# Kernel tuning notes

Hardware: AMD Instinct MI355X
Metric: run time of the kernel (lower is better)

The kernel has to match this reference:

```python
import jax, jax.numpy as jnp
import numpy as np

CHUNK = 1024  # chunk over N to avoid materializing the full [B,N,M] distance matrix


def _min_dists(xyz1, xyz2):
    """For each point in xyz1 [B,N,3], squared L2 distance to nearest point in xyz2 [B,M,3].
    Returns [B,N]. Computed in chunks of N to bound peak memory."""
    B, N, _ = xyz1.shape
    y2 = jnp.sum(xyz2 * xyz2, axis=-1)  # [B,M]
    n_chunks = N // CHUNK
    # [n_chunks, B, CHUNK, 3]
    xc = jnp.transpose(xyz1.reshape(B, n_chunks, CHUNK, 3), (1, 0, 2, 3))

    def chunk_min(x):  # x: [B,CHUNK,3]
        x2 = jnp.sum(x * x, axis=-1)  # [B,CHUNK]
        xy = jnp.einsum('bcd,bmd->bcm', x, xyz2)  # [B,CHUNK,M]
        d = x2[:, :, None] + y2[:, None, :] - 2.0 * xy
        return jnp.min(d, axis=-1)  # [B,CHUNK]

    mins = jax.lax.map(chunk_min, xc)  # [n_chunks, B, CHUNK]
    return jnp.transpose(mins, (1, 0, 2)).reshape(B, N)


def setup_inputs() -> dict:
    key = jax.random.key(0)
    k1, k2 = jax.random.split(key)
    xyz1 = jax.random.normal(k1, (8, 8192, 3), dtype=jnp.float32)
    xyz2 = jax.random.normal(k2, (8, 8192, 3), dtype=jnp.float32)
    return {"xyz1": xyz1, "xyz2": xyz2}


def reference(xyz1, xyz2):
    # ChamferDistanceL2.forward with ignore_zeros=False and batch>1:
    # only dist1 (xyz1 -> nearest in xyz2) is used; return its mean.
    dist1 = _min_dists(xyz1, xyz2)  # [B,N]
    return jnp.mean(dist1)
```

## Files before the change

kernel.cpp:

```cpp
#include <hip/hip_runtime.h>

typedef _Float16 v8h __attribute__((ext_vector_type(8)));
typedef float v16f __attribute__((ext_vector_type(16)));

#define BB 8
#define NN 8192
#define MM 8192
#define SPLITM 8
#define JT_PER_CHUNK 32
#define NI 2
#define TPB 256

#define AFRAG_OFF 0
#define BFRAG_OFF (8 * 256 * 64 * 16)
#define PMINS_OFF (2 * BFRAG_OFF)


__global__ __launch_bounds__(256) void pack_a(const float* __restrict__ xyz2,
                                              v8h* __restrict__ afrag,
                                              float* __restrict__ out) {
    int gid = blockIdx.x * 256 + threadIdx.x;
    if (gid == 0) out[0] = 0.0f;
    int lane = gid & 63;
    int jt = (gid >> 6) & 255;
    int b = gid >> 14;
    int j = jt * 32 + (lane & 31);
    int khalf = lane >> 5;
    const float* p = xyz2 + ((size_t)b * MM + j) * 3;
    _Float16 h0 = (_Float16)p[0], h1 = (_Float16)p[1], h2 = (_Float16)p[2];
    float y0 = (float)h0, y1 = (float)h1, y2v = (float)h2;
    float s = fmaf(y0, y0, fmaf(y1, y1, y2v * y2v));
    _Float16 shi = (_Float16)s;
    _Float16 slo = (_Float16)(s - (float)shi);
    v8h v = {0, 0, 0, 0, 0, 0, 0, 0};
    if (khalf == 0) {
        v[0] = h0; v[1] = h1; v[2] = h2;
        v[3] = shi; v[4] = slo;
        v[5] = (_Float16)1.0f; v[6] = (_Float16)1.0f;
    }
    afrag[gid] = v;
}

__global__ __launch_bounds__(256) void pack_b(const float* __restrict__ xyz1,
                                              v8h* __restrict__ bfrag) {
    int gid = blockIdx.x * 256 + threadIdx.x;
    int lane = gid & 63;
    int it = (gid >> 6) & 255;
    int b = gid >> 14;
    int i = it * 32 + (lane & 31);
    int khalf = lane >> 5;
    const float* p = xyz1 + ((size_t)b * NN + i) * 3;
    _Float16 h0 = (_Float16)p[0], h1 = (_Float16)p[1], h2 = (_Float16)p[2];
    float x0 = (float)h0, x1 = (float)h1, x2v = (float)h2;
    float s = fmaf(x0, x0, fmaf(x1, x1, x2v * x2v));
    _Float16 shi = (_Float16)s;
    _Float16 slo = (_Float16)(s - (float)shi);
    v8h v = {0, 0, 0, 0, 0, 0, 0, 0};
    if (khalf == 0) {
        v[0] = (_Float16)(-2.0f * x0);
        v[1] = (_Float16)(-2.0f * x1);
        v[2] = (_Float16)(-2.0f * x2v);
        v[3] = (_Float16)1.0f; v[4] = (_Float16)1.0f;
        v[5] = shi; v[6] = slo;
    }
    bfrag[gid] = v;
}

__global__ __launch_bounds__(TPB, 4) void chamfer_min_mfma(const v8h* __restrict__ afrag,
                                                           const v8h* __restrict__ bfrag,
                                                           float* __restrict__ pmins) {
    __shared__ v8h aLds[JT_PER_CHUNK * 64];

    int ig4    = blockIdx.x & 31;
    int jchunk = (blockIdx.x >> 5) & 7;
    int b      = blockIdx.x >> 8;
    int wid  = threadIdx.x >> 6;
    int lane = threadIdx.x & 63;

    {
        const uint4* src = (const uint4*)(afrag + ((size_t)b * 256 + jchunk * JT_PER_CHUNK) * 64);
        uint4* dst = (uint4*)aLds;
#pragma unroll
        for (int r = 0; r < JT_PER_CHUNK * 64 / TPB; ++r)
            dst[r * TPB + threadIdx.x] = src[r * TPB + threadIdx.x];
    }

    int it0 = (ig4 * 4 + wid) * NI;
    v8h b0 = bfrag[((size_t)b * 256 + it0 + 0) * 64 + lane];
    v8h b1 = bfrag[((size_t)b * 256 + it0 + 1) * 64 + lane];

    __syncthreads();

    const v16f zc = {0, 0, 0, 0, 0, 0, 0, 0, 0, 0, 0, 0, 0, 0, 0, 0};
    float m0 = 1e30f, m1 = 1e30f;

#pragma unroll 2
    for (int jt = 0; jt < JT_PER_CHUNK; ++jt) {
        v8h a = aLds[jt * 64 + lane];
        v16f c0 = __builtin_amdgcn_mfma_f32_32x32x16_f16(a, b0, zc, 0, 0, 0);
        v16f c1 = __builtin_amdgcn_mfma_f32_32x32x16_f16(a, b1, zc, 0, 0, 0);
#pragma unroll
        for (int r = 0; r < 16; r += 4) {
            m0 = fminf(m0, fminf(fminf(c0[r], c0[r + 1]), fminf(c0[r + 2], c0[r + 3])));
            m1 = fminf(m1, fminf(fminf(c1[r], c1[r + 1]), fminf(c1[r + 2], c1[r + 3])));
        }
    }

    m0 = fminf(m0, __shfl_xor(m0, 32));
    m1 = fminf(m1, __shfl_xor(m1, 32));

    int half = lane >> 5;
    int i = (it0 + half) * 32 + (lane & 31);
    float mv = half ? m1 : m0;
    pmins[(size_t)jchunk * (BB * NN) + (size_t)b * NN + i] = mv;
}

__global__ __launch_bounds__(256) void chamfer_reduce(const float* __restrict__ pmins,
                                                      float* __restrict__ out) {
    int i = blockIdx.x * 256 + threadIdx.x;
    float m = pmins[i];
#pragma unroll
    for (int sp = 1; sp < SPLITM; ++sp)
        m = fminf(m, pmins[(size_t)sp * (BB * NN) + i]);
    float s = m;
#pragma unroll
    for (int off = 32; off > 0; off >>= 1) s += __shfl_down(s, off);
    __shared__ float ls[4];
    int lane = threadIdx.x & 63, wv = threadIdx.x >> 6;
    if (lane == 0) ls[wv] = s;
    __syncthreads();
    if (threadIdx.x == 0) {
        float t = (ls[0] + ls[1]) + (ls[2] + ls[3]);
        atomicAdd(out, t * (1.0f / (float)(BB * NN)));
    }
}

extern "C" void kernel_launch(void* const* d_in, const int* in_sizes, int n_in,
                              void* d_out, int out_size, void* d_ws, size_t ws_size,
                              hipStream_t stream) {
    const float* xyz1 = (const float*)d_in[0];
    const float* xyz2 = (const float*)d_in[1];
    float* out = (float*)d_out;
    v8h* afrag = (v8h*)((char*)d_ws + AFRAG_OFF);
    v8h* bfrag = (v8h*)((char*)d_ws + BFRAG_OFF);
    float* pmins = (float*)((char*)d_ws + PMINS_OFF);

    pack_a<<<(BB * 256 * 64) / 256, 256, 0, stream>>>(xyz2, afrag, out);
    pack_b<<<(BB * 256 * 64) / 256, 256, 0, stream>>>(xyz1, bfrag);
    chamfer_min_mfma<<<BB * SPLITM * 32, TPB, 0, stream>>>(afrag, bfrag, pmins);
    chamfer_reduce<<<(BB * NN) / 256, 256, 0, stream>>>(pmins, out);
}
```

Measured before the change: 87.34 us.

## Fuse packing, MFMA min search and reduction into a single mega-kernel

```diff
diff --git a/kernel.cpp b/kernel.cpp
--- a/kernel.cpp
+++ b/kernel.cpp
@@ -6,133 +6,128 @@
 #define BB 8
 #define NN 8192
 #define MM 8192
-#define SPLITM 8
-#define JT_PER_CHUNK 32
-#define NI 2
-#define TPB 256
-
-#define AFRAG_OFF 0
-#define BFRAG_OFF (8 * 256 * 64 * 16)
-#define PMINS_OFF (2 * BFRAG_OFF)
+#define NCHUNK 8
+#define JTC 32
+#define CPTS (JTC * 32)
+#define TPB 128
+#define PPT (CPTS / TPB)
 
 
-__global__ __launch_bounds__(256) void pack_a(const float* __restrict__ xyz2,
-                                              v8h* __restrict__ afrag,
-                                              float* __restrict__ out) {
-    int gid = blockIdx.x * 256 + threadIdx.x;
-    if (gid == 0) out[0] = 0.0f;
-    int lane = gid & 63;
-    int jt = (gid >> 6) & 255;
-    int b = gid >> 14;
-    int j = jt * 32 + (lane & 31);
-    int khalf = lane >> 5;
-    const float* p = xyz2 + ((size_t)b * MM + j) * 3;
-    _Float16 h0 = (_Float16)p[0], h1 = (_Float16)p[1], h2 = (_Float16)p[2];
+__device__ __forceinline__ v8h cvt_a(float x, float y, float z) {
+    _Float16 h0 = (_Float16)x, h1 = (_Float16)y, h2 = (_Float16)z;
     float y0 = (float)h0, y1 = (float)h1, y2v = (float)h2;
     float s = fmaf(y0, y0, fmaf(y1, y1, y2v * y2v));
     _Float16 shi = (_Float16)s;
     _Float16 slo = (_Float16)(s - (float)shi);
-    v8h v = {0, 0, 0, 0, 0, 0, 0, 0};
-    if (khalf == 0) {
-        v[0] = h0; v[1] = h1; v[2] = h2;
-        v[3] = shi; v[4] = slo;
-        v[5] = (_Float16)1.0f; v[6] = (_Float16)1.0f;
-    }
-    afrag[gid] = v;
+    v8h v = {h0, h1, h2, shi, slo, (_Float16)1.0f, (_Float16)1.0f, (_Float16)0.0f};
+    return v;
 }
 
-__global__ __launch_bounds__(256) void pack_b(const float* __restrict__ xyz1,
-                                              v8h* __restrict__ bfrag) {
-    int gid = blockIdx.x * 256 + threadIdx.x;
-    int lane = gid & 63;
-    int it = (gid >> 6) & 255;
-    int b = gid >> 14;
-    int i = it * 32 + (lane & 31);
-    int khalf = lane >> 5;
-    const float* p = xyz1 + ((size_t)b * NN + i) * 3;
-    _Float16 h0 = (_Float16)p[0], h1 = (_Float16)p[1], h2 = (_Float16)p[2];
-    float x0 = (float)h0, x1 = (float)h1, x2v = (float)h2;
-    float s = fmaf(x0, x0, fmaf(x1, x1, x2v * x2v));
-    _Float16 shi = (_Float16)s;
-    _Float16 slo = (_Float16)(s - (float)shi);
-    v8h v = {0, 0, 0, 0, 0, 0, 0, 0};
-    if (khalf == 0) {
-        v[0] = (_Float16)(-2.0f * x0);
-        v[1] = (_Float16)(-2.0f * x1);
-        v[2] = (_Float16)(-2.0f * x2v);
-        v[3] = (_Float16)1.0f; v[4] = (_Float16)1.0f;
-        v[5] = shi; v[6] = slo;
-    }
-    bfrag[gid] = v;
-}
+__global__ __launch_bounds__(TPB, 1) void chamfer_mega(const float* __restrict__ xyz1,
+                                                       const float* __restrict__ xyz2,
+                                                       float* __restrict__ out) {
+    __shared__ v8h aLds[2][JTC * 64];
+    __shared__ float ls[2];
 
-__global__ __launch_bounds__(TPB, 4) void chamfer_min_mfma(const v8h* __restrict__ afrag,
-                                                           const v8h* __restrict__ bfrag,
-                                                           float* __restrict__ pmins) {
-    __shared__ v8h aLds[JT_PER_CHUNK * 64];
-
-    int ig4    = blockIdx.x & 31;
-    int jchunk = (blockIdx.x >> 5) & 7;
-    int b      = blockIdx.x >> 8;
-    int wid  = threadIdx.x >> 6;
-    int lane = threadIdx.x & 63;
+    int ig = blockIdx.x & 63;
+    int b  = blockIdx.x >> 6;
+    int t  = threadIdx.x;
+    int wid = t >> 6;
+    int lane = t & 63;
+    int laneq = lane & 31;
+    int half = lane >> 5;
 
     {
-        const uint4* src = (const uint4*)(afrag + ((size_t)b * 256 + jchunk * JT_PER_CHUNK) * 64);
-        uint4* dst = (uint4*)aLds;
+        v8h z = {};
 #pragma unroll
-        for (int r = 0; r < JT_PER_CHUNK * 64 / TPB; ++r)
-            dst[r * TPB + threadIdx.x] = src[r * TPB + threadIdx.x];
+        for (int r = 0; r < 16; ++r) {
+            int s = r * TPB + t;
+            int buf = s >> 10;
+            int jt  = (s >> 5) & 31;
+            int sl  = s & 31;
+            aLds[buf][jt * 64 + 32 + sl] = z;
+        }
     }
 
-    int it0 = (ig4 * 4 + wid) * NI;
-    v8h b0 = bfrag[((size_t)b * 256 + it0 + 0) * 64 + lane];
-    v8h b1 = bfrag[((size_t)b * 256 + it0 + 1) * 64 + lane];
+    int it0 = (ig * 2 + wid) * 2;
+    v8h bf0, bf1;
+#pragma unroll
+    for (int tt = 0; tt < 2; ++tt) {
+        int i = (it0 + tt) * 32 + laneq;
+        const float* p = xyz1 + ((size_t)b * NN + i) * 3;
+        _Float16 h0 = (_Float16)p[0], h1 = (_Float16)p[1], h2 = (_Float16)p[2];
+        float x0 = (float)h0, x1 = (float)h1, x2v = (float)h2;
+        float s = fmaf(x0, x0, fmaf(x1, x1, x2v * x2v));
+        _Float16 shi = (_Float16)s;
+        _Float16 slo = (_Float16)(s - (float)shi);
+        v8h v = {};
+        if (half == 0) {
+            v[0] = (_Float16)(-2.0f * x0);
+            v[1] = (_Float16)(-2.0f * x1);
+            v[2] = (_Float16)(-2.0f * x2v);
+            v[3] = (_Float16)1.0f; v[4] = (_Float16)1.0f;
+            v[5] = shi; v[6] = slo;
+        }
+        if (tt == 0) bf0 = v; else bf1 = v;
+    }
 
+    const float* xb = xyz2 + (size_t)b * MM * 3;
+    float4 pr[6];
+    {
+        const float4* src = (const float4*)(xb + (size_t)t * PPT * 3);
+#pragma unroll
+        for (int r = 0; r < 6; ++r) pr[r] = src[r];
+        const float* fl = (const float*)pr;
+#pragma unroll
+        for (int k = 0; k < PPT; ++k) {
+            int p = t * PPT + k;
+            aLds[0][(p >> 5) * 64 + (p & 31)] = cvt_a(fl[3 * k], fl[3 * k + 1], fl[3 * k + 2]);
+        }
+    }
     __syncthreads();
 
-    const v16f zc = {0, 0, 0, 0, 0, 0, 0, 0, 0, 0, 0, 0, 0, 0, 0, 0};
+    const v16f zc = {};
     float m0 = 1e30f, m1 = 1e30f;
-
-#pragma unroll 2
-    for (int jt = 0; jt < JT_PER_CHUNK; ++jt) {
-        v8h a = aLds[jt * 64 + lane];
-        v16f c0 = __builtin_amdgcn_mfma_f32_32x32x16_f16(a, b0, zc, 0, 0, 0);
-        v16f c1 = __builtin_amdgcn_mfma_f32_32x32x16_f16(a, b1, zc, 0, 0, 0);
+#pragma unroll 1
+    for (int c = 0; c < NCHUNK; ++c) {
+        int cb = c & 1;
+        if (c + 1 < NCHUNK) {
+            const float4* src = (const float4*)(xb + ((size_t)(c + 1) * CPTS + (size_t)t * PPT) * 3);
 #pragma unroll
-        for (int r = 0; r < 16; r += 4) {
-            m0 = fminf(m0, fminf(fminf(c0[r], c0[r + 1]), fminf(c0[r + 2], c0[r + 3])));
-            m1 = fminf(m1, fminf(fminf(c1[r], c1[r + 1]), fminf(c1[r + 2], c1[r + 3])));
+            for (int r = 0; r < 6; ++r) pr[r] = src[r];
         }
+#pragma unroll 4
+        for (int jt = 0; jt < JTC; ++jt) {
+            v8h a = aLds[cb][jt * 64 + lane];
+            v16f c0 = __builtin_amdgcn_mfma_f32_32x32x16_f16(a, bf0, zc, 0, 0, 0);
+            v16f c1 = __builtin_amdgcn_mfma_f32_32x32x16_f16(a, bf1, zc, 0, 0, 0);
+#pragma unroll
+            for (int r = 0; r < 16; r += 4) {
+                m0 = fminf(m0, fminf(fminf(c0[r], c0[r + 1]), fminf(c0[r + 2], c0[r + 3])));
+                m1 = fminf(m1, fminf(fminf(c1[r], c1[r + 1]), fminf(c1[r + 2], c1[r + 3])));
+            }
+        }
+        if (c + 1 < NCHUNK) {
+            const float* fl = (const float*)pr;
+#pragma unroll
+            for (int k = 0; k < PPT; ++k) {
+                int p = t * PPT + k;
+                aLds[cb ^ 1][(p >> 5) * 64 + (p & 31)] = cvt_a(fl[3 * k], fl[3 * k + 1], fl[3 * k + 2]);
+            }
+        }
+        __syncthreads();
     }
 
     m0 = fminf(m0, __shfl_xor(m0, 32));
     m1 = fminf(m1, __shfl_xor(m1, 32));
+    float mv = half ? m1 : m0;
 
-    int half = lane >> 5;
-    int i = (it0 + half) * 32 + (lane & 31);
-    float mv = half ? m1 : m0;
-    pmins[(size_t)jchunk * (BB * NN) + (size_t)b * NN + i] = mv;
-}
-
-__global__ __launch_bounds__(256) void chamfer_reduce(const float* __restrict__ pmins,
-                                                      float* __restrict__ out) {
-    int i = blockIdx.x * 256 + threadIdx.x;
-    float m = pmins[i];
-#pragma unroll
-    for (int sp = 1; sp < SPLITM; ++sp)
-        m = fminf(m, pmins[(size_t)sp * (BB * NN) + i]);
-    float s = m;
+    float s = mv;
 #pragma unroll
     for (int off = 32; off > 0; off >>= 1) s += __shfl_down(s, off);
-    __shared__ float ls[4];
-    int lane = threadIdx.x & 63, wv = threadIdx.x >> 6;
-    if (lane == 0) ls[wv] = s;
+    if (lane == 0) ls[wid] = s;
     __syncthreads();
-    if (threadIdx.x == 0) {
-        float t = (ls[0] + ls[1]) + (ls[2] + ls[3]);
-        atomicAdd(out, t * (1.0f / (float)(BB * NN)));
-    }
+    if (t == 0) atomicAdd(out, (ls[0] + ls[1]) * (1.0f / (float)(BB * NN)));
 }
 
 extern "C" void kernel_launch(void* const* d_in, const int* in_sizes, int n_in,
@@ -141,12 +136,7 @@
     const float* xyz1 = (const float*)d_in[0];
     const float* xyz2 = (const float*)d_in[1];
     float* out = (float*)d_out;
-    v8h* afrag = (v8h*)((char*)d_ws + AFRAG_OFF);
-    v8h* bfrag = (v8h*)((char*)d_ws + BFRAG_OFF);
-    float* pmins = (float*)((char*)d_ws + PMINS_OFF);
 
-    pack_a<<<(BB * 256 * 64) / 256, 256, 0, stream>>>(xyz2, afrag, out);
-    pack_b<<<(BB * 256 * 64) / 256, 256, 0, stream>>>(xyz1, bfrag);
-    chamfer_min_mfma<<<BB * SPLITM * 32, TPB, 0, stream>>>(afrag, bfrag, pmins);
-    chamfer_reduce<<<(BB * NN) / 256, 256, 0, stream>>>(pmins, out);
+    hipMemsetAsync(out, 0, sizeof(float), stream);
+    chamfer_mega<<<BB * 64, TPB, 0, stream>>>(xyz1, xyz2, out);
 }
```

Measured after the change: 108.6 us. 24.4% more time.
